# Kernel optimization log

Hardware: AMD Instinct MI355X
Metric: run time of the kernel (lower is better)

Reference implementation:

```python
import jax, jax.numpy as jnp
import numpy as np

N_NODES = 50000
N_EDGES = 800000
N_GRAPHS = 128
IN_DIM, HID_DIM, OUT_DIM = 128, 96, 10


def setup_inputs() -> dict:
    key = jax.random.key(0)
    ks = jax.random.split(key, 9)
    x = jax.random.normal(ks[0], (N_NODES, IN_DIM), dtype=jnp.float32)
    edge_index = jax.random.randint(ks[1], (2, N_EDGES), 0, N_NODES, dtype=jnp.int32)
    batch = jnp.sort(jax.random.randint(ks[2], (N_NODES,), 0, N_GRAPHS, dtype=jnp.int32))
    s1 = 1.0 / np.sqrt(IN_DIM)
    s2 = 1.0 / np.sqrt(HID_DIM)
    W1 = jax.random.uniform(ks[3], (IN_DIM, HID_DIM), jnp.float32, -s1, s1)
    b1 = jnp.zeros((HID_DIM,), jnp.float32)
    W2 = jax.random.uniform(ks[4], (HID_DIM, HID_DIM), jnp.float32, -s2, s2)
    b2 = jnp.zeros((HID_DIM,), jnp.float32)
    Wf = jax.random.uniform(ks[5], (OUT_DIM, HID_DIM), jnp.float32, -s2, s2)
    bf = jax.random.uniform(ks[6], (OUT_DIM,), jnp.float32, -s2, s2)
    return {"x": x, "edge_index": edge_index, "batch": batch,
            "W1": W1, "b1": b1, "W2": W2, "b2": b2, "Wf": Wf, "bf": bf}


def reference(x, edge_index, batch, W1, b1, W2, b2, Wf, bf):
    n = x.shape[0]
    row, col = edge_index[0], edge_index[1]
    # GCN symmetric normalization with self-loops: deg = 1 + in-degree
    deg = jax.ops.segment_sum(jnp.ones_like(col, dtype=x.dtype), col, num_segments=n) + 1.0
    dinv = deg ** -0.5  # [N]
    norm = dinv[row] * dinv[col]  # [E]

    def gcn_conv(h, W, b):
        h = h @ W  # [N, F_out]
        # edge messages: norm_e * h[src] scattered to dst; self-loops handled analytically
        agg = jax.ops.segment_sum(norm[:, None] * h[row], col, num_segments=n)
        agg = agg + (dinv * dinv)[:, None] * h
        return agg + b

    h = jax.nn.relu(gcn_conv(x, W1, b1))
    h = gcn_conv(h, W2, b2)

    # global mean pool over graphs
    counts = jax.ops.segment_sum(jnp.ones((n,), x.dtype), batch, num_segments=N_GRAPHS)
    pooled = jax.ops.segment_sum(h, batch, num_segments=N_GRAPHS)
    pooled = pooled / jnp.maximum(counts, 1.0)[:, None]

    logits = pooled @ Wf.T + bf
    return jax.nn.log_softmax(logits, axis=1)
```

## Files before the change

kernel.cpp:

```cpp
#include <hip/hip_runtime.h>
#include <hip/hip_bf16.h>

#define N_GRAPHS 128
#define HID 96
#define OUT_DIM 10
#define CAP 64

typedef __attribute__((ext_vector_type(8))) short short8;
typedef __attribute__((ext_vector_type(4))) float f32x4;
typedef __attribute__((ext_vector_type(2))) float f32x2;

__device__ inline unsigned short f2bf(float f) {
    union { float f; unsigned u; } x;
    x.f = f;
    unsigned r = x.u + 0x7FFFu + ((x.u >> 16) & 1u);
    return (unsigned short)(r >> 16);
}

__device__ inline unsigned char f2fp8(float v) {
    int p = __builtin_amdgcn_cvt_pk_fp8_f32(v, v, 0, false);
    return (unsigned char)(p & 0xff);
}

__device__ inline void unpack8_fp8(uint2 v, float* o) {
    f32x2 a = __builtin_amdgcn_cvt_pk_f32_fp8((int)v.x, false);
    f32x2 b = __builtin_amdgcn_cvt_pk_f32_fp8((int)v.x, true);
    f32x2 c = __builtin_amdgcn_cvt_pk_f32_fp8((int)v.y, false);
    f32x2 d = __builtin_amdgcn_cvt_pk_f32_fp8((int)v.y, true);
    o[0] = a.x; o[1] = a.y; o[2] = b.x; o[3] = b.y;
    o[4] = c.x; o[5] = c.y; o[6] = d.x; o[7] = d.y;
}

__global__ __launch_bounds__(256) void fill_kernel(const int* __restrict__ rowi,
                                                   const int* __restrict__ coli,
                                                   int* __restrict__ cnt,
                                                   unsigned short* __restrict__ srcs,
                                                   int E, int N) {
    const int part = blockIdx.x & 7;
    const int chunk = blockIdx.x >> 3;
    const int base = chunk * 2048;
    const int plo = (int)(((long long)N * part) >> 3);
    const int phi = (int)(((long long)N * (part + 1)) >> 3);
#pragma unroll
    for (int it = 0; it < 8; ++it) {
        int e = base + it * 256 + threadIdx.x;
        if (e < E) {
            int c = coli[e];
            if (c >= plo && c < phi) {
                int pos = atomicAdd(&cnt[c], 1);
                if (pos < CAP) srcs[(size_t)c * CAP + pos] = (unsigned short)rowi[e];
            }
        }
    }
}

template <int K, bool IN_BF16>
__global__ __launch_bounds__(256) void gemm_mfma(const void* __restrict__ Xv,
                                                 const float* __restrict__ W,
                                                 const int* __restrict__ cnt,
                                                 unsigned char* __restrict__ Tp, int N) {
    constexpr int P = K + 8;
    constexpr int KT = K / 32;
    __shared__ __align__(16) unsigned short Wt[96 * P];
    const int tid = threadIdx.x;
    const int row0 = blockIdx.x * 64;

    for (int idx = tid; idx < K * 96; idx += 256) {
        int k = idx / 96, n = idx - k * 96;
        Wt[n * P + k] = f2bf(W[idx]);
    }
    __syncthreads();

    const int wv = tid >> 6;
    const int lane = tid & 63;
    const int m = lane & 15;
    const int quad = lane >> 4;
    const int row = row0 + wv * 16 + m;

    short8 afrag[KT];
    if (row < N) {
        if (IN_BF16) {
            const unsigned short* Xr = (const unsigned short*)Xv + (size_t)row * K;
#pragma unroll
            for (int t = 0; t < KT; ++t) afrag[t] = *(const short8*)(Xr + t * 32 + quad * 8);
        } else {
            const float* Xr = (const float*)Xv + (size_t)row * K;
#pragma unroll
            for (int t = 0; t < KT; ++t) {
                float4 a0 = *(const float4*)(Xr + t * 32 + quad * 8);
                float4 a1 = *(const float4*)(Xr + t * 32 + quad * 8 + 4);
                short8 a;
                a[0] = (short)f2bf(a0.x); a[1] = (short)f2bf(a0.y);
                a[2] = (short)f2bf(a0.z); a[3] = (short)f2bf(a0.w);
                a[4] = (short)f2bf(a1.x); a[5] = (short)f2bf(a1.y);
                a[6] = (short)f2bf(a1.z); a[7] = (short)f2bf(a1.w);
                afrag[t] = a;
            }
        }
    } else {
#pragma unroll
        for (int t = 0; t < KT; ++t) afrag[t] = short8{0, 0, 0, 0, 0, 0, 0, 0};
    }

    f32x4 acc[6];
#pragma unroll
    for (int nt = 0; nt < 6; ++nt) acc[nt] = f32x4{0.f, 0.f, 0.f, 0.f};
#pragma unroll
    for (int t = 0; t < KT; ++t) {
#pragma unroll
        for (int nt = 0; nt < 6; ++nt) {
            short8 bfrag = *(const short8*)&Wt[(nt * 16 + m) * P + t * 32 + quad * 8];
            acc[nt] = __builtin_amdgcn_mfma_f32_16x16x32_bf16(afrag[t], bfrag, acc[nt], 0, 0, 0);
        }
    }
#pragma unroll
    for (int r = 0; r < 4; ++r) {
        int orow = row0 + wv * 16 + quad * 4 + r;
        if (orow < N) {
            float d = rsqrtf(1.0f + (float)cnt[orow]);
#pragma unroll
            for (int nt = 0; nt < 6; ++nt)
                Tp[(size_t)orow * 96 + nt * 16 + m] = f2fp8(d * acc[nt][r]);
        }
    }
}

__global__ void gather1_kernel(const unsigned char* __restrict__ Tp,
                               const unsigned short* __restrict__ srcs,
                               const int* __restrict__ cnt, const float* __restrict__ b,
                               unsigned short* __restrict__ H, int N) {
    int gid = blockIdx.x * 256 + threadIdx.x;
    if (gid >= N * 12) return;
    int i = gid / 12;
    int j = gid - i * 12;
    const uint2* Trow = (const uint2*)Tp;

    int ci = cnt[i];
    float di = rsqrtf(1.0f + (float)ci);
    float acc[8], tmp[8];
    unpack8_fp8(Trow[(size_t)i * 12 + j], acc);

    int e = min(ci, CAP);
    const unsigned short* sp = srcs + (size_t)i * CAP;
    int k = 0;
    for (; k + 4 <= e; k += 4) {
        ushort4 s4 = *(const ushort4*)(sp + k);
        uint2 v0 = Trow[(size_t)s4.x * 12 + j];
        uint2 v1 = Trow[(size_t)s4.y * 12 + j];
        uint2 v2 = Trow[(size_t)s4.z * 12 + j];
        uint2 v3 = Trow[(size_t)s4.w * 12 + j];
        unpack8_fp8(v0, tmp);
#pragma unroll
        for (int l = 0; l < 8; ++l) acc[l] += tmp[l];
        unpack8_fp8(v1, tmp);
#pragma unroll
        for (int l = 0; l < 8; ++l) acc[l] += tmp[l];
        unpack8_fp8(v2, tmp);
#pragma unroll
        for (int l = 0; l < 8; ++l) acc[l] += tmp[l];
        unpack8_fp8(v3, tmp);
#pragma unroll
        for (int l = 0; l < 8; ++l) acc[l] += tmp[l];
    }
    for (; k < e; ++k) {
        unpack8_fp8(Trow[(size_t)sp[k] * 12 + j], tmp);
#pragma unroll
        for (int l = 0; l < 8; ++l) acc[l] += tmp[l];
    }

    unsigned short o[8];
#pragma unroll
    for (int l = 0; l < 8; ++l) {
        float v = fmaxf(di * acc[l] + b[j * 8 + l], 0.0f);
        o[l] = f2bf(v);
    }
    uint4 pk;
    pk.x = (unsigned)o[0] | ((unsigned)o[1] << 16);
    pk.y = (unsigned)o[2] | ((unsigned)o[3] << 16);
    pk.z = (unsigned)o[4] | ((unsigned)o[5] << 16);
    pk.w = (unsigned)o[6] | ((unsigned)o[7] << 16);
    ((uint4*)H)[(size_t)i * 12 + j] = pk;
}

__global__ __launch_bounds__(192) void gather2_pool(const unsigned char* __restrict__ Tp,
                                                    const unsigned short* __restrict__ srcs,
                                                    const int* __restrict__ cnt,
                                                    const int* __restrict__ batch,
                                                    float* __restrict__ pooled, int N) {
    __shared__ float hl[16 * 96];
    __shared__ int g_l[16];
    const int tid = threadIdx.x;
    const int n = tid / 12;
    const int j = tid - n * 12;
    const int i = blockIdx.x * 16 + n;
    if (tid < 16) {
        int ii = blockIdx.x * 16 + tid;
        g_l[tid] = (ii < N) ? batch[ii] : -1;
    }

    float acc[8] = {0.f, 0.f, 0.f, 0.f, 0.f, 0.f, 0.f, 0.f};
    float di = 0.0f;
    if (i < N) {
        const uint2* Trow = (const uint2*)Tp;
        int ci = cnt[i];
        di = rsqrtf(1.0f + (float)ci);
        float tmp[8];
        unpack8_fp8(Trow[(size_t)i * 12 + j], acc);
        int e = min(ci, CAP);
        const unsigned short* sp = srcs + (size_t)i * CAP;
        int k = 0;
        for (; k + 4 <= e; k += 4) {
            ushort4 s4 = *(const ushort4*)(sp + k);
            uint2 v0 = Trow[(size_t)s4.x * 12 + j];
            uint2 v1 = Trow[(size_t)s4.y * 12 + j];
            uint2 v2 = Trow[(size_t)s4.z * 12 + j];
            uint2 v3 = Trow[(size_t)s4.w * 12 + j];
            unpack8_fp8(v0, tmp);
#pragma unroll
            for (int l = 0; l < 8; ++l) acc[l] += tmp[l];
            unpack8_fp8(v1, tmp);
#pragma unroll
            for (int l = 0; l < 8; ++l) acc[l] += tmp[l];
            unpack8_fp8(v2, tmp);
#pragma unroll
            for (int l = 0; l < 8; ++l) acc[l] += tmp[l];
            unpack8_fp8(v3, tmp);
#pragma unroll
            for (int l = 0; l < 8; ++l) acc[l] += tmp[l];
        }
        for (; k < e; ++k) {
            unpack8_fp8(Trow[(size_t)sp[k] * 12 + j], tmp);
#pragma unroll
            for (int l = 0; l < 8; ++l) acc[l] += tmp[l];
        }
    }
#pragma unroll
    for (int l = 0; l < 8; ++l) hl[n * 96 + j * 8 + l] = di * acc[l];
    __syncthreads();

    if (tid < 96) {
        int f = tid;
        float s = 0.0f;
        int gcur = -2;
        for (int nn = 0; nn < 16; ++nn) {
            int g = g_l[nn];
            if (g < 0) continue;
            if (g != gcur) {
                if (gcur >= 0) atomicAdd(&pooled[gcur * 96 + f], s);
                gcur = g;
                s = 0.0f;
            }
            s += hl[nn * 96 + f];
        }
        if (gcur >= 0) atomicAdd(&pooled[gcur * 96 + f], s);
    }
}

__device__ inline int lower_bound_dev(const int* __restrict__ a, int n, int val) {
    int lo = 0, hi = n;
    while (lo < hi) {
        int m = (lo + hi) >> 1;
        if (a[m] < val) lo = m + 1; else hi = m;
    }
    return lo;
}

__global__ void head_kernel(const float* __restrict__ pooled, const int* __restrict__ batch,
                            const float* __restrict__ b2, const float* __restrict__ Wf,
                            const float* __restrict__ bfv, float* __restrict__ out, int N) {
    __shared__ float wfs[OUT_DIM * HID];
    __shared__ float b2s[HID];
    __shared__ float bfs[OUT_DIM];
    int t = threadIdx.x;
    for (int idx = t; idx < OUT_DIM * HID; idx += 128) wfs[idx] = Wf[idx];
    if (t < HID) b2s[t] = b2[t];
    if (t < OUT_DIM) bfs[t] = bfv[t];
    __syncthreads();
    int g = t;
    if (g >= N_GRAPHS) return;
    int lo = lower_bound_dev(batch, N, g);
    int hi = lower_bound_dev(batch, N, g + 1);
    int c = hi - lo;
    float inv = (c > 0) ? 1.0f / (float)c : 0.0f;
    float hasb = (c > 0) ? 1.0f : 0.0f;
    float logits[OUT_DIM];
#pragma unroll
    for (int o = 0; o < OUT_DIM; ++o) {
        float s = 0.0f;
        for (int cc = 0; cc < HID; ++cc)
            s += (pooled[g * HID + cc] * inv + hasb * b2s[cc]) * wfs[o * HID + cc];
        logits[o] = s + bfs[o];
    }
    float m = logits[0];
#pragma unroll
    for (int o = 1; o < OUT_DIM; ++o) m = fmaxf(m, logits[o]);
    float se = 0.0f;
#pragma unroll
    for (int o = 0; o < OUT_DIM; ++o) se += expf(logits[o] - m);
    float lse = m + logf(se);
#pragma unroll
    for (int o = 0; o < OUT_DIM; ++o) out[g * OUT_DIM + o] = logits[o] - lse;
}

extern "C" void kernel_launch(void* const* d_in, const int* in_sizes, int n_in,
                              void* d_out, int out_size, void* d_ws, size_t ws_size,
                              hipStream_t stream) {
    const float* x     = (const float*)d_in[0];
    const int*   ei    = (const int*)d_in[1];
    const int*   batch = (const int*)d_in[2];
    const float* W1    = (const float*)d_in[3];
    const float* b1    = (const float*)d_in[4];
    const float* W2    = (const float*)d_in[5];
    const float* b2    = (const float*)d_in[6];
    const float* Wf    = (const float*)d_in[7];
    const float* bf    = (const float*)d_in[8];

    const int N = in_sizes[0] / 128;
    const int E = in_sizes[1] / 2;
    const int* rowi = ei;
    const int* coli = ei + E;

    size_t off = 0;
    auto alloc = [&](size_t bytes) {
        void* p = (char*)d_ws + off;
        off += (bytes + 255) & ~(size_t)255;
        return p;
    };
    int*            cnt    = (int*)alloc((size_t)N * 4);
    unsigned short* srcs   = (unsigned short*)alloc((size_t)N * CAP * 2);
    unsigned char*  Tp     = (unsigned char*)alloc((size_t)N * HID);
    unsigned short* H      = (unsigned short*)alloc((size_t)N * HID * 2);
    float*          pooled = (float*)alloc((size_t)N_GRAPHS * HID * 4);

    hipMemsetAsync(cnt, 0, (size_t)N * 4, stream);
    hipMemsetAsync(pooled, 0, (size_t)N_GRAPHS * HID * 4, stream);

    const int nchunk = (E + 2047) / 2048;
    fill_kernel<<<nchunk * 8, 256, 0, stream>>>(rowi, coli, cnt, srcs, E, N);

    gemm_mfma<128, false><<<(N + 63) / 64, 256, 0, stream>>>(x, W1, cnt, Tp, N);
    gather1_kernel<<<(N * 12 + 255) / 256, 256, 0, stream>>>(Tp, srcs, cnt, b1, H, N);

    gemm_mfma<96, true><<<(N + 63) / 64, 256, 0, stream>>>(H, W2, cnt, Tp, N);
    gather2_pool<<<(N + 15) / 16, 192, 0, stream>>>(Tp, srcs, cnt, batch, pooled, N);

    head_kernel<<<1, 128, 0, stream>>>(pooled, batch, b2, Wf, bf, (float*)d_out, N);
}
```

Before: 214.4 us.

## Fuse layer-1 gather with layer-2 GEMM and widen gather loads to 16 bytes

Layer 1's neighbour aggregation now writes its bf16 hidden tile straight into shared memory, and the layer-2 MFMA GEMM consumes it in the same kernel. This removes the global H round trip and one launch. Both gather kernels now load 16 fp8 values per thread (uint4) instead of 8, so each node uses 6 threads and a block covers more nodes. The two memsets become one by placing cnt and pooled next to each other. In exchange, each fused block has fewer threads gathering per node and uses more shared memory, which may lower occupancy and latency hiding in the irregular gather.

```diff
diff --git a/kernel.cpp b/kernel.cpp
--- a/kernel.cpp
+++ b/kernel.cpp
@@ -22,13 +22,19 @@
     return (unsigned char)(p & 0xff);
 }
 
-__device__ inline void unpack8_fp8(uint2 v, float* o) {
-    f32x2 a = __builtin_amdgcn_cvt_pk_f32_fp8((int)v.x, false);
-    f32x2 b = __builtin_amdgcn_cvt_pk_f32_fp8((int)v.x, true);
-    f32x2 c = __builtin_amdgcn_cvt_pk_f32_fp8((int)v.y, false);
-    f32x2 d = __builtin_amdgcn_cvt_pk_f32_fp8((int)v.y, true);
-    o[0] = a.x; o[1] = a.y; o[2] = b.x; o[3] = b.y;
-    o[4] = c.x; o[5] = c.y; o[6] = d.x; o[7] = d.y;
+__device__ inline void unpack16_fp8(uint4 v, float* o) {
+    f32x2 a0 = __builtin_amdgcn_cvt_pk_f32_fp8((int)v.x, false);
+    f32x2 a1 = __builtin_amdgcn_cvt_pk_f32_fp8((int)v.x, true);
+    f32x2 b0 = __builtin_amdgcn_cvt_pk_f32_fp8((int)v.y, false);
+    f32x2 b1 = __builtin_amdgcn_cvt_pk_f32_fp8((int)v.y, true);
+    f32x2 c0 = __builtin_amdgcn_cvt_pk_f32_fp8((int)v.z, false);
+    f32x2 c1 = __builtin_amdgcn_cvt_pk_f32_fp8((int)v.z, true);
+    f32x2 d0 = __builtin_amdgcn_cvt_pk_f32_fp8((int)v.w, false);
+    f32x2 d1 = __builtin_amdgcn_cvt_pk_f32_fp8((int)v.w, true);
+    o[0] = a0.x;  o[1] = a0.y;  o[2] = a1.x;  o[3] = a1.y;
+    o[4] = b0.x;  o[5] = b0.y;  o[6] = b1.x;  o[7] = b1.y;
+    o[8] = c0.x;  o[9] = c0.y;  o[10] = c1.x; o[11] = c1.y;
+    o[12] = d0.x; o[13] = d0.y; o[14] = d1.x; o[15] = d1.y;
 }
 
 __global__ __launch_bounds__(256) void fill_kernel(const int* __restrict__ rowi,
@@ -54,11 +60,11 @@
     }
 }
 
-template <int K, bool IN_BF16>
-__global__ __launch_bounds__(256) void gemm_mfma(const void* __restrict__ Xv,
-                                                 const float* __restrict__ W,
-                                                 const int* __restrict__ cnt,
-                                                 unsigned char* __restrict__ Tp, int N) {
+__global__ __launch_bounds__(256) void gemm1_mfma(const float* __restrict__ X,
+                                                  const float* __restrict__ W,
+                                                  const int* __restrict__ cnt,
+                                                  unsigned char* __restrict__ Tp, int N) {
+    constexpr int K = 128;
     constexpr int P = K + 8;
     constexpr int KT = K / 32;
     __shared__ __align__(16) unsigned short Wt[96 * P];
@@ -79,23 +85,17 @@
 
     short8 afrag[KT];
     if (row < N) {
-        if (IN_BF16) {
-            const unsigned short* Xr = (const unsigned short*)Xv + (size_t)row * K;
-#pragma unroll
-            for (int t = 0; t < KT; ++t) afrag[t] = *(const short8*)(Xr + t * 32 + quad * 8);
-        } else {
-            const float* Xr = (const float*)Xv + (size_t)row * K;
-#pragma unroll
-            for (int t = 0; t < KT; ++t) {
-                float4 a0 = *(const float4*)(Xr + t * 32 + quad * 8);
-                float4 a1 = *(const float4*)(Xr + t * 32 + quad * 8 + 4);
-                short8 a;
-                a[0] = (short)f2bf(a0.x); a[1] = (short)f2bf(a0.y);
-                a[2] = (short)f2bf(a0.z); a[3] = (short)f2bf(a0.w);
-                a[4] = (short)f2bf(a1.x); a[5] = (short)f2bf(a1.y);
-                a[6] = (short)f2bf(a1.z); a[7] = (short)f2bf(a1.w);
-                afrag[t] = a;
-            }
+        const float* Xr = X + (size_t)row * K;
+#pragma unroll
+        for (int t = 0; t < KT; ++t) {
+            float4 a0 = *(const float4*)(Xr + t * 32 + quad * 8);
+            float4 a1 = *(const float4*)(Xr + t * 32 + quad * 8 + 4);
+            short8 a;
+            a[0] = (short)f2bf(a0.x); a[1] = (short)f2bf(a0.y);
+            a[2] = (short)f2bf(a0.z); a[3] = (short)f2bf(a0.w);
+            a[4] = (short)f2bf(a1.x); a[5] = (short)f2bf(a1.y);
+            a[6] = (short)f2bf(a1.z); a[7] = (short)f2bf(a1.w);
+            afrag[t] = a;
         }
     } else {
 #pragma unroll
@@ -125,61 +125,108 @@
     }
 }
 
-__global__ void gather1_kernel(const unsigned char* __restrict__ Tp,
-                               const unsigned short* __restrict__ srcs,
-                               const int* __restrict__ cnt, const float* __restrict__ b,
-                               unsigned short* __restrict__ H, int N) {
-    int gid = blockIdx.x * 256 + threadIdx.x;
-    if (gid >= N * 12) return;
-    int i = gid / 12;
-    int j = gid - i * 12;
-    const uint2* Trow = (const uint2*)Tp;
-
-    int ci = cnt[i];
-    float di = rsqrtf(1.0f + (float)ci);
-    float acc[8], tmp[8];
-    unpack8_fp8(Trow[(size_t)i * 12 + j], acc);
-
-    int e = min(ci, CAP);
-    const unsigned short* sp = srcs + (size_t)i * CAP;
-    int k = 0;
-    for (; k + 4 <= e; k += 4) {
-        ushort4 s4 = *(const ushort4*)(sp + k);
-        uint2 v0 = Trow[(size_t)s4.x * 12 + j];
-        uint2 v1 = Trow[(size_t)s4.y * 12 + j];
-        uint2 v2 = Trow[(size_t)s4.z * 12 + j];
-        uint2 v3 = Trow[(size_t)s4.w * 12 + j];
-        unpack8_fp8(v0, tmp);
-#pragma unroll
-        for (int l = 0; l < 8; ++l) acc[l] += tmp[l];
-        unpack8_fp8(v1, tmp);
-#pragma unroll
-        for (int l = 0; l < 8; ++l) acc[l] += tmp[l];
-        unpack8_fp8(v2, tmp);
-#pragma unroll
-        for (int l = 0; l < 8; ++l) acc[l] += tmp[l];
-        unpack8_fp8(v3, tmp);
-#pragma unroll
-        for (int l = 0; l < 8; ++l) acc[l] += tmp[l];
-    }
-    for (; k < e; ++k) {
-        unpack8_fp8(Trow[(size_t)sp[k] * 12 + j], tmp);
-#pragma unroll
-        for (int l = 0; l < 8; ++l) acc[l] += tmp[l];
-    }
-
-    unsigned short o[8];
-#pragma unroll
-    for (int l = 0; l < 8; ++l) {
-        float v = fmaxf(di * acc[l] + b[j * 8 + l], 0.0f);
-        o[l] = f2bf(v);
-    }
-    uint4 pk;
-    pk.x = (unsigned)o[0] | ((unsigned)o[1] << 16);
-    pk.y = (unsigned)o[2] | ((unsigned)o[3] << 16);
-    pk.z = (unsigned)o[4] | ((unsigned)o[5] << 16);
-    pk.w = (unsigned)o[6] | ((unsigned)o[7] << 16);
-    ((uint4*)H)[(size_t)i * 12 + j] = pk;
+__global__ __launch_bounds__(256) void gather1_gemm2(const unsigned char* __restrict__ Tp1,
+                                                     const unsigned short* __restrict__ srcs,
+                                                     const int* __restrict__ cnt,
+                                                     const float* __restrict__ b1,
+                                                     const float* __restrict__ W2,
+                                                     unsigned char* __restrict__ Tp2, int N) {
+    constexpr int PH = 104;
+    constexpr int PW = 104;
+    __shared__ __align__(16) unsigned short Hs[128 * PH];
+    __shared__ __align__(16) unsigned short Wt[96 * PW];
+    const int tid = threadIdx.x;
+    const int node0 = blockIdx.x * 128;
+
+    for (int idx = tid; idx < 96 * 96; idx += 256) {
+        int k = idx / 96, n = idx - k * 96;
+        Wt[n * PW + k] = f2bf(W2[idx]);
+    }
+
+    const uint4* Trow = (const uint4*)Tp1;
+#pragma unroll
+    for (int it = 0; it < 3; ++it) {
+        int idx = it * 256 + tid;
+        int n = idx / 6, j = idx - n * 6;
+        int i = node0 + n;
+        if (i < N) {
+            float acc[16], tmp[16];
+            unpack16_fp8(Trow[(size_t)i * 6 + j], acc);
+            int ci = cnt[i];
+            int e = min(ci, CAP);
+            const unsigned short* sp = srcs + (size_t)i * CAP;
+            int k = 0;
+            for (; k + 4 <= e; k += 4) {
+                ushort4 s4 = *(const ushort4*)(sp + k);
+                uint4 v0 = Trow[(size_t)s4.x * 6 + j];
+                uint4 v1 = Trow[(size_t)s4.y * 6 + j];
+                uint4 v2 = Trow[(size_t)s4.z * 6 + j];
+                uint4 v3 = Trow[(size_t)s4.w * 6 + j];
+                unpack16_fp8(v0, tmp);
+#pragma unroll
+                for (int l = 0; l < 16; ++l) acc[l] += tmp[l];
+                unpack16_fp8(v1, tmp);
+#pragma unroll
+                for (int l = 0; l < 16; ++l) acc[l] += tmp[l];
+                unpack16_fp8(v2, tmp);
+#pragma unroll
+                for (int l = 0; l < 16; ++l) acc[l] += tmp[l];
+                unpack16_fp8(v3, tmp);
+#pragma unroll
+                for (int l = 0; l < 16; ++l) acc[l] += tmp[l];
+            }
+            for (; k < e; ++k) {
+                unpack16_fp8(Trow[(size_t)sp[k] * 6 + j], tmp);
+#pragma unroll
+                for (int l = 0; l < 16; ++l) acc[l] += tmp[l];
+            }
+            float di = rsqrtf(1.0f + (float)ci);
+#pragma unroll
+            for (int l = 0; l < 16; ++l) {
+                float v = fmaxf(di * acc[l] + b1[j * 16 + l], 0.0f);
+                Hs[n * PH + j * 16 + l] = f2bf(v);
+            }
+        } else {
+#pragma unroll
+            for (int l = 0; l < 16; ++l) Hs[n * PH + j * 16 + l] = 0;
+        }
+    }
+    __syncthreads();
+
+    const int wv = tid >> 6;
+    const int lane = tid & 63;
+    const int m = lane & 15;
+    const int quad = lane >> 4;
+#pragma unroll
+    for (int half = 0; half < 2; ++half) {
+        const int rt = wv + half * 4;
+        const int lrow = rt * 16 + m;
+        short8 afrag[3];
+#pragma unroll
+        for (int t = 0; t < 3; ++t)
+            afrag[t] = *(const short8*)&Hs[lrow * PH + t * 32 + quad * 8];
+        f32x4 acc[6];
+#pragma unroll
+        for (int nt = 0; nt < 6; ++nt) acc[nt] = f32x4{0.f, 0.f, 0.f, 0.f};
+#pragma unroll
+        for (int t = 0; t < 3; ++t) {
+#pragma unroll
+            for (int nt = 0; nt < 6; ++nt) {
+                short8 bfrag = *(const short8*)&Wt[(nt * 16 + m) * PW + t * 32 + quad * 8];
+                acc[nt] = __builtin_amdgcn_mfma_f32_16x16x32_bf16(afrag[t], bfrag, acc[nt], 0, 0, 0);
+            }
+        }
+#pragma unroll
+        for (int r = 0; r < 4; ++r) {
+            int orow = node0 + rt * 16 + quad * 4 + r;
+            if (orow < N) {
+                float d = rsqrtf(1.0f + (float)cnt[orow]);
+#pragma unroll
+                for (int nt = 0; nt < 6; ++nt)
+                    Tp2[(size_t)orow * 96 + nt * 16 + m] = f2fp8(d * acc[nt][r]);
+            }
+        }
+    }
 }
 
 __global__ __launch_bounds__(192) void gather2_pool(const unsigned char* __restrict__ Tp,
@@ -187,62 +234,64 @@
                                                     const int* __restrict__ cnt,
                                                     const int* __restrict__ batch,
                                                     float* __restrict__ pooled, int N) {
-    __shared__ float hl[16 * 96];
-    __shared__ int g_l[16];
+    __shared__ float hl[32 * 96];
+    __shared__ int g_l[32];
     const int tid = threadIdx.x;
-    const int n = tid / 12;
-    const int j = tid - n * 12;
-    const int i = blockIdx.x * 16 + n;
-    if (tid < 16) {
-        int ii = blockIdx.x * 16 + tid;
+    const int n = tid / 6;
+    const int j = tid - n * 6;
+    const int i = blockIdx.x * 32 + n;
+    if (tid < 32) {
+        int ii = blockIdx.x * 32 + tid;
         g_l[tid] = (ii < N) ? batch[ii] : -1;
     }
 
-    float acc[8] = {0.f, 0.f, 0.f, 0.f, 0.f, 0.f, 0.f, 0.f};
+    float acc[16];
+#pragma unroll
+    for (int l = 0; l < 16; ++l) acc[l] = 0.0f;
     float di = 0.0f;
     if (i < N) {
-        const uint2* Trow = (const uint2*)Tp;
+        const uint4* Trow = (const uint4*)Tp;
+        float tmp[16];
+        unpack16_fp8(Trow[(size_t)i * 6 + j], acc);
         int ci = cnt[i];
         di = rsqrtf(1.0f + (float)ci);
-        float tmp[8];
-        unpack8_fp8(Trow[(size_t)i * 12 + j], acc);
         int e = min(ci, CAP);
         const unsigned short* sp = srcs + (size_t)i * CAP;
         int k = 0;
         for (; k + 4 <= e; k += 4) {
             ushort4 s4 = *(const ushort4*)(sp + k);
-            uint2 v0 = Trow[(size_t)s4.x * 12 + j];
-            uint2 v1 = Trow[(size_t)s4.y * 12 + j];
-            uint2 v2 = Trow[(size_t)s4.z * 12 + j];
-            uint2 v3 = Trow[(size_t)s4.w * 12 + j];
-            unpack8_fp8(v0, tmp);
-#pragma unroll
-            for (int l = 0; l < 8; ++l) acc[l] += tmp[l];
-            unpack8_fp8(v1, tmp);
-#pragma unroll
-            for (int l = 0; l < 8; ++l) acc[l] += tmp[l];
-            unpack8_fp8(v2, tmp);
-#pragma unroll
-            for (int l = 0; l < 8; ++l) acc[l] += tmp[l];
-            unpack8_fp8(v3, tmp);
-#pragma unroll
-            for (int l = 0; l < 8; ++l) acc[l] += tmp[l];
+            uint4 v0 = Trow[(size_t)s4.x * 6 + j];
+            uint4 v1 = Trow[(size_t)s4.y * 6 + j];
+            uint4 v2 = Trow[(size_t)s4.z * 6 + j];
+            uint4 v3 = Trow[(size_t)s4.w * 6 + j];
+            unpack16_fp8(v0, tmp);
+#pragma unroll
+            for (int l = 0; l < 16; ++l) acc[l] += tmp[l];
+            unpack16_fp8(v1, tmp);
+#pragma unroll
+            for (int l = 0; l < 16; ++l) acc[l] += tmp[l];
+            unpack16_fp8(v2, tmp);
+#pragma unroll
+            for (int l = 0; l < 16; ++l) acc[l] += tmp[l];
+            unpack16_fp8(v3, tmp);
+#pragma unroll
+            for (int l = 0; l < 16; ++l) acc[l] += tmp[l];
         }
         for (; k < e; ++k) {
-            unpack8_fp8(Trow[(size_t)sp[k] * 12 + j], tmp);
-#pragma unroll
-            for (int l = 0; l < 8; ++l) acc[l] += tmp[l];
-        }
-    }
-#pragma unroll
-    for (int l = 0; l < 8; ++l) hl[n * 96 + j * 8 + l] = di * acc[l];
+            unpack16_fp8(Trow[(size_t)sp[k] * 6 + j], tmp);
+#pragma unroll
+            for (int l = 0; l < 16; ++l) acc[l] += tmp[l];
+        }
+    }
+#pragma unroll
+    for (int l = 0; l < 16; ++l) hl[n * 96 + j * 16 + l] = di * acc[l];
     __syncthreads();
 
     if (tid < 96) {
         int f = tid;
         float s = 0.0f;
         int gcur = -2;
-        for (int nn = 0; nn < 16; ++nn) {
+        for (int nn = 0; nn < 32; ++nn) {
             int g = g_l[nn];
             if (g < 0) continue;
             if (g != gcur) {
@@ -327,22 +376,22 @@
         return p;
     };
     int*            cnt    = (int*)alloc((size_t)N * 4);
+    float*          pooled = (float*)alloc((size_t)N_GRAPHS * HID * 4);
+    size_t zero_bytes = off;
     unsigned short* srcs   = (unsigned short*)alloc((size_t)N * CAP * 2);
-    unsigned char*  Tp     = (unsigned char*)alloc((size_t)N * HID);
-    unsigned short* H      = (unsigned short*)alloc((size_t)N * HID * 2);
-    float*          pooled = (float*)alloc((size_t)N_GRAPHS * HID * 4);
-
-    hipMemsetAsync(cnt, 0, (size_t)N * 4, stream);
-    hipMemsetAsync(pooled, 0, (size_t)N_GRAPHS * HID * 4, stream);
+    unsigned char*  Tp1    = (unsigned char*)alloc((size_t)N * HID);
+    unsigned char*  Tp2    = (unsigned char*)alloc((size_t)N * HID);
+
+    hipMemsetAsync(d_ws, 0, zero_bytes, stream);
 
     const int nchunk = (E + 2047) / 2048;
     fill_kernel<<<nchunk * 8, 256, 0, stream>>>(rowi, coli, cnt, srcs, E, N);
 
-    gemm_mfma<128, false><<<(N + 63) / 64, 256, 0, stream>>>(x, W1, cnt, Tp, N);
-    gather1_kernel<<<(N * 12 + 255) / 256, 256, 0, stream>>>(Tp, srcs, cnt, b1, H, N);
-
-    gemm_mfma<96, true><<<(N + 63) / 64, 256, 0, stream>>>(H, W2, cnt, Tp, N);
-    gather2_pool<<<(N + 15) / 16, 192, 0, stream>>>(Tp, srcs, cnt, batch, pooled, N);
+    gemm1_mfma<<<(N + 63) / 64, 256, 0, stream>>>(x, W1, cnt, Tp1, N);
+
+    gather1_gemm2<<<(N + 127) / 128, 256, 0, stream>>>(Tp1, srcs, cnt, b1, W2, Tp2, N);
+
+    gather2_pool<<<(N + 31) / 32, 192, 0, stream>>>(Tp2, srcs, cnt, batch, pooled, N);
 
     head_kernel<<<1, 128, 0, stream>>>(pooled, batch, b2, Wf, bf, (float*)d_out, N);
 }
```

After: 213.7 us, median of 2. About the same (-0.3%).
